# Optimization experiments

Measured on AMD Instinct MI355X. Metric: run time of the kernel, lower is better.

Reference implementation:

```python
import jax, jax.numpy as jnp
import numpy as np

NUM_HEADS = 8


def setup_inputs() -> dict:
    key = jax.random.key(0)
    ks = jax.random.split(key, 8)
    B, C, H, W = 8, 512, 64, 64
    s = 1.0 / np.sqrt(C)
    return {
        "guide": jax.random.normal(ks[0], (B, C), dtype=jnp.float32),
        "hidden_rep": jax.random.normal(ks[1], (B, C, H, W), dtype=jnp.float32),
        "Wq": jax.random.normal(ks[2], (C, C), dtype=jnp.float32) * s,
        "bq": jnp.zeros((C,), dtype=jnp.float32),
        "Wk": jax.random.normal(ks[3], (C, C), dtype=jnp.float32) * s,
        "bk": jnp.zeros((C,), dtype=jnp.float32),
        "Wv": jax.random.normal(ks[4], (C, C), dtype=jnp.float32) * s,
        "bv": jnp.zeros((C,), dtype=jnp.float32),
    }


def reference(guide, hidden_rep, Wq, bq, Wk, bk, Wv, bv):
    B, C, H, W = hidden_rep.shape
    nh = NUM_HEADS
    d = C // nh
    scale = 1.0 / (d ** 0.5)

    # hidden_rep: [B,C,H,W] -> [B, HW, C] (token-major, matching torch permute+reshape)
    hr = hidden_rep.transpose(0, 2, 3, 1).reshape(B, H * W, C)

    # guide is broadcast identically over all HW positions in the original;
    # the linear commutes with the broadcast, so compute once then broadcast.
    q_row = guide @ Wq.T + bq                                   # [B, C]
    q_tok = jnp.broadcast_to(q_row[:, None, :], (B, H * W, C))  # [B, HW, C]
    k_tok = hr @ Wk.T + bk                                      # [B, HW, C]
    v_tok = hr @ Wv.T + bv                                      # [B, HW, C]

    # Faithful replication of torch split_heads: view [B,HW,C] as [B,nh,d,H,W]
    # (this scrambles spatial/channel axes exactly as the original does),
    # then permute to [B, nh, H, W, d].
    def split_heads(x):
        return x.reshape(B, nh, d, H, W).transpose(0, 1, 3, 4, 2)

    q = split_heads(q_tok)  # [B, nh, H, W, d]
    k = split_heads(k_tok)
    v = split_heads(v_tok)

    # Row-wise attention: softmax over the width axis only.
    scores = jnp.einsum('bnhqd,bnhkd->bnhqk', q, k) * scale  # [B, nh, H, W, W]
    weights = jax.nn.softmax(scores, axis=-1)
    attended = jnp.einsum('bnhqk,bnhkd->bnhqd', weights, v)  # [B, nh, H, W, d]

    # permute(0,1,4,2,3) -> [B, nh, d, H, W] -> [B, C, H, W]
    return attended.transpose(0, 1, 4, 2, 3).reshape(B, C, H, W)
```

## Files before the change

### kernel.cpp

```cpp
#include <hip/hip_runtime.h>
#include <hip/hip_bf16.h>
#include <stdint.h>


typedef __attribute__((ext_vector_type(8))) short bf16x8_t;
typedef __attribute__((ext_vector_type(4))) float f32x4_t;

__device__ __forceinline__ unsigned short f2bf(float f) {
  unsigned int u = __float_as_uint(f);
  u += 0x7FFFu + ((u >> 16) & 1u);
  return (unsigned short)(u >> 16);
}

__device__ __forceinline__ void gload16(const unsigned short* g, void* lds) {
  __builtin_amdgcn_global_load_lds(
      (const __attribute__((address_space(1))) unsigned int*)g,
      (__attribute__((address_space(3))) unsigned int*)lds, 16, 0, 0);
}

__global__ __launch_bounds__(256) void k_wvb(const float* __restrict__ Wv,
                                             unsigned short* __restrict__ Wvb) {
  int gid = blockIdx.x * 256 + threadIdx.x;
  float4 v = ((const float4*)Wv)[gid];
  ushort4 o;
  o.x = f2bf(v.x); o.y = f2bf(v.y); o.z = f2bf(v.z); o.w = f2bf(v.w);
  ((ushort4*)Wvb)[gid] = o;
}

__global__ __launch_bounds__(256) void k_trans(const float* __restrict__ hid,
                                               unsigned short* __restrict__ XT,
                                               float* __restrict__ hrsum) {
  int bid = blockIdx.x;
  int cb = bid & 7, n = (bid >> 3) & 7, b = bid >> 6;
  int tid = threadIdx.x;
  __shared__ float T[64][65];
  __shared__ float hsred[64][8];

  for (int i = tid; i < 512; i += 256) ((float*)hsred)[i] = 0.f;

  float part[4][4];
#pragma unroll
  for (int m = 0; m < 4; ++m)
#pragma unroll
    for (int i = 0; i < 4; ++i) part[m][i] = 0.f;

  const int f4 = tid & 15;
  const int r0 = tid >> 4;
  const float* srcbase = hid + (size_t)(b * 512 + cb * 64) * 4096 + n * 512;
  unsigned short* xtbase = XT + (size_t)(b * 8 + n) * 512 * 512 + cb * 64;

  for (int jc = 0; jc < 8; ++jc) {
    __syncthreads();
#pragma unroll
    for (int m = 0; m < 4; ++m) {
      int r = r0 + 16 * m;
      float4 v = *(const float4*)(srcbase + (size_t)r * 4096 + jc * 64 + f4 * 4);
      T[r][f4 * 4 + 0] = v.x;  T[r][f4 * 4 + 1] = v.y;
      T[r][f4 * 4 + 2] = v.z;  T[r][f4 * 4 + 3] = v.w;
      part[m][0] += v.x; part[m][1] += v.y; part[m][2] += v.z; part[m][3] += v.w;
    }
    __syncthreads();
#pragma unroll
    for (int p = 0; p < 2; ++p) {
      int jl = (tid >> 3) + p * 32;
      int o = tid & 7;
      unsigned short t0 = f2bf(T[o * 8 + 0][jl]);
      unsigned short t1 = f2bf(T[o * 8 + 1][jl]);
      unsigned short t2 = f2bf(T[o * 8 + 2][jl]);
      unsigned short t3 = f2bf(T[o * 8 + 3][jl]);
      unsigned short t4 = f2bf(T[o * 8 + 4][jl]);
      unsigned short t5 = f2bf(T[o * 8 + 5][jl]);
      unsigned short t6 = f2bf(T[o * 8 + 6][jl]);
      unsigned short t7 = f2bf(T[o * 8 + 7][jl]);
      uint4 pk;
      pk.x = (unsigned)t0 | ((unsigned)t1 << 16);
      pk.y = (unsigned)t2 | ((unsigned)t3 << 16);
      pk.z = (unsigned)t4 | ((unsigned)t5 << 16);
      pk.w = (unsigned)t6 | ((unsigned)t7 << 16);
      *(uint4*)(xtbase + (size_t)(jc * 64 + jl) * 512 + o * 8) = pk;
    }
  }
  __syncthreads();
  {
    int gbase = (tid & 1) * 4;
#pragma unroll
    for (int m = 0; m < 4; ++m) {
      int r = r0 + 16 * m;
#pragma unroll
      for (int i = 0; i < 4; ++i) atomicAdd(&hsred[r][gbase + i], part[m][i]);
    }
  }
  __syncthreads();
  float* hout = hrsum + (size_t)(b * 8 + n) * 8 * 512 + cb * 64;
  for (int i = tid; i < 512; i += 256) {
    int g = i >> 6, r = i & 63;
    hout[(size_t)g * 512 + r] = hsred[r][g];
  }
}

__global__ __launch_bounds__(256) void k_k2(const float* __restrict__ hrsum,
                                            const float* __restrict__ Wk,
                                            const float* __restrict__ bk,
                                            const float* __restrict__ guide,
                                            const float* __restrict__ Wq,
                                            const float* __restrict__ bq,
                                            float* __restrict__ K2,
                                            float* __restrict__ qs) {
  int bid = blockIdx.x;
  int rt = bid >> 4, ct = bid & 15;
  bool isQ = (rt == 16);
  const float* A = isQ ? guide : (hrsum + (size_t)rt * 32 * 512);
  const float* Bm = isQ ? Wq : Wk;
  int arows = isQ ? 8 : 32;
  int tid = threadIdx.x;
  __shared__ float Ah[32][36];
  __shared__ float Bh[32][36];
  int r = tid >> 3, f = tid & 7;
  int oy = (tid >> 4) * 2, ox = (tid & 15) * 2;
  float a00 = 0.f, a01 = 0.f, a10 = 0.f, a11 = 0.f;

  for (int kc = 0; kc < 16; ++kc) {
    __syncthreads();
    float4 av = (r < arows) ? *(const float4*)(A + (size_t)r * 512 + kc * 32 + f * 4)
                            : make_float4(0.f, 0.f, 0.f, 0.f);
    *(float4*)(&Ah[r][f * 4]) = av;
    float4 bv = *(const float4*)(Bm + (size_t)(ct * 32 + r) * 512 + kc * 32 + f * 4);
    *(float4*)(&Bh[r][f * 4]) = bv;
    __syncthreads();
#pragma unroll
    for (int kk = 0; kk < 32; kk += 4) {
      float4 x0 = *(float4*)(&Ah[oy][kk]);
      float4 x1 = *(float4*)(&Ah[oy + 1][kk]);
      float4 y0 = *(float4*)(&Bh[ox][kk]);
      float4 y1 = *(float4*)(&Bh[ox + 1][kk]);
      a00 += x0.x * y0.x + x0.y * y0.y + x0.z * y0.z + x0.w * y0.w;
      a01 += x0.x * y1.x + x0.y * y1.y + x0.z * y1.z + x0.w * y1.w;
      a10 += x1.x * y0.x + x1.y * y0.y + x1.z * y0.z + x1.w * y0.w;
      a11 += x1.x * y1.x + x1.y * y1.y + x1.z * y1.z + x1.w * y1.w;
    }
  }
  int c0 = ct * 32 + ox;
  if (!isQ) {
    int row0 = rt * 32 + oy;
    K2[(size_t)row0 * 512 + c0]           = a00 + 64.f * bk[c0];
    K2[(size_t)row0 * 512 + c0 + 1]       = a01 + 64.f * bk[c0 + 1];
    K2[(size_t)(row0 + 1) * 512 + c0]     = a10 + 64.f * bk[c0];
    K2[(size_t)(row0 + 1) * 512 + c0 + 1] = a11 + 64.f * bk[c0 + 1];
  } else if (oy < 8) {
    const float scale = 0.125f;
    qs[(size_t)oy * 512 + c0]           = (a00 + bq[c0]) * scale;
    qs[(size_t)oy * 512 + c0 + 1]       = (a01 + bq[c0 + 1]) * scale;
    qs[(size_t)(oy + 1) * 512 + c0]     = (a10 + bq[c0]) * scale;
    qs[(size_t)(oy + 1) * 512 + c0 + 1] = (a11 + bq[c0 + 1]) * scale;
  }
}

__global__ __launch_bounds__(512, 4) void k_fused(
    const unsigned short* __restrict__ XT, const unsigned short* __restrict__ Wvb,
    const float* __restrict__ K2, const float* __restrict__ qs,
    const float* __restrict__ bv, float* __restrict__ out) {
  int bid = blockIdx.x;
  int g = bid & 7, slab = bid >> 3;
  int n = slab & 7, b = slab >> 3;
  int tid = threadIdx.x;
  int w = tid >> 6, l = tid & 63;
  int l15 = l & 15, l4 = l >> 4, lr = l >> 3, lc = l & 7;

  __shared__ __align__(16) unsigned char smem[77824];
  unsigned char* Al = smem;
  unsigned char* Bl = smem + 65536;
  float* K2l = (float*)(smem + 73728);
  float* bvl = (float*)(smem + 75776);

  if (tid < 128) {
    ((float4*)K2l)[tid] = ((const float4*)(K2 + (size_t)(slab * 8 + g) * 512))[tid];
  } else if (tid < 256) {
    ((float4*)bvl)[tid - 128] = ((const float4*)bv)[tid - 128];
  }

  const unsigned swzel = (unsigned)(lc ^ lr) << 3;
  const unsigned short* bsrc = XT + (size_t)slab * 512 * 512;

  f32x4_t acc[4][4];
#pragma unroll
  for (int i = 0; i < 4; ++i)
#pragma unroll
    for (int j = 0; j < 4; ++j) acc[i][j] = (f32x4_t){0.f, 0.f, 0.f, 0.f};

  const int myArow = w * 64;
  const int myBrow = w * 8;

  for (int kc = 0; kc < 8; ++kc) {
    if (kc) __syncthreads();
#pragma unroll
    for (int i = 0; i < 8; ++i) {
      int r = myArow + i * 8 + lr;
      gload16(Wvb + (size_t)r * 512 + kc * 64 + swzel, Al + (myArow + i * 8) * 128);
    }
    {
      int r = myBrow + lr;
      int j = 8 * r + g;
      gload16(bsrc + (size_t)j * 512 + kc * 64 + swzel, Bl + myBrow * 128);
    }
    __syncthreads();
#pragma unroll
    for (int ks = 0; ks < 2; ++ks) {
      unsigned colb = (unsigned)(ks * 64 + l4 * 16);
      bf16x8_t af[4], bfr[4];
#pragma unroll
      for (int mt = 0; mt < 4; ++mt) {
        unsigned row = (unsigned)(myArow + mt * 16 + l15);
        af[mt] = *(const bf16x8_t*)(Al + row * 128 + (colb ^ ((row & 7) << 4)));
      }
#pragma unroll
      for (int nt = 0; nt < 4; ++nt) {
        unsigned row = (unsigned)(nt * 16 + l15);
        bfr[nt] = *(const bf16x8_t*)(Bl + row * 128 + (colb ^ ((row & 7) << 4)));
      }
#pragma unroll
      for (int mt = 0; mt < 4; ++mt)
#pragma unroll
        for (int nt = 0; nt < 4; ++nt)
          acc[mt][nt] = __builtin_amdgcn_mfma_f32_16x16x32_bf16(
              af[mt], bfr[nt], acc[mt][nt], 0, 0, 0);
    }
  }

  __syncthreads();
  unsigned char* Vl = Al;
#pragma unroll
  for (int nt = 0; nt < 4; ++nt) {
    unsigned dd = (unsigned)(nt * 16 + l15);
    unsigned swz = (dd & 7) << 4;
#pragma unroll
    for (int mt = 0; mt < 4; ++mt) {
      int c0 = w * 64 + mt * 16 + l4 * 4;
      float4 bq4 = *(const float4*)(bvl + c0);
      float v0 = acc[mt][nt][0] + bq4.x;
      float v1 = acc[mt][nt][1] + bq4.y;
      float v2 = acc[mt][nt][2] + bq4.z;
      float v3 = acc[mt][nt][3] + bq4.w;
      uint2 pk;
      pk.x = (unsigned)f2bf(v0) | ((unsigned)f2bf(v1) << 16);
      pk.y = (unsigned)f2bf(v2) | ((unsigned)f2bf(v3) << 16);
      *(uint2*)(Vl + dd * 1024 + (((unsigned)(c0 * 2)) ^ swz)) = pk;
    }
  }
  __syncthreads();

  const int e = w;
  float alpha = qs[(size_t)b * 512 + e * 64 + l];
  float mmax = -3.0e38f;
#pragma unroll 8
  for (int kk = 0; kk < 64; ++kk)
    mmax = fmaxf(mmax, alpha * K2l[e * 64 + kk]);
  float ssum = 0.f;
#pragma unroll 8
  for (int kk = 0; kk < 64; ++kk)
    ssum += __expf(alpha * K2l[e * 64 + kk] - mmax);
  float inv = 1.0f / ssum;

  f32x4_t acc2[4][4];
#pragma unroll
  for (int i = 0; i < 4; ++i)
#pragma unroll
    for (int j = 0; j < 4; ++j) acc2[i][j] = (f32x4_t){0.f, 0.f, 0.f, 0.f};

#pragma unroll
  for (int ks = 0; ks < 2; ++ks) {
    bf16x8_t va[4];
#pragma unroll
    for (int mt = 0; mt < 4; ++mt) {
      unsigned dd = (unsigned)(mt * 16 + l15);
      unsigned colb = (unsigned)(e * 128 + ks * 64 + l4 * 16);
      va[mt] = *(const bf16x8_t*)(Vl + dd * 1024 + (colb ^ ((dd & 7) << 4)));
    }
    int kk0 = ks * 32 + l4 * 8;
    float4 be0 = *(float4*)(&K2l[e * 64 + kk0]);
    float4 be1 = *(float4*)(&K2l[e * 64 + kk0 + 4]);
    bf16x8_t pb[4];
#pragma unroll
    for (int nt = 0; nt < 4; ++nt) {
      int qq = nt * 16 + l15;
      float aq = __shfl(alpha, qq);
      float mq = __shfl(mmax, qq);
      float iq = __shfl(inv, qq);
      bf16x8_t p;
      p[0] = (short)f2bf(__expf(aq * be0.x - mq) * iq);
      p[1] = (short)f2bf(__expf(aq * be0.y - mq) * iq);
      p[2] = (short)f2bf(__expf(aq * be0.z - mq) * iq);
      p[3] = (short)f2bf(__expf(aq * be0.w - mq) * iq);
      p[4] = (short)f2bf(__expf(aq * be1.x - mq) * iq);
      p[5] = (short)f2bf(__expf(aq * be1.y - mq) * iq);
      p[6] = (short)f2bf(__expf(aq * be1.z - mq) * iq);
      p[7] = (short)f2bf(__expf(aq * be1.w - mq) * iq);
      pb[nt] = p;
    }
#pragma unroll
    for (int mt = 0; mt < 4; ++mt)
#pragma unroll
      for (int nt = 0; nt < 4; ++nt)
        acc2[mt][nt] = __builtin_amdgcn_mfma_f32_16x16x32_bf16(
            va[mt], pb[nt], acc2[mt][nt], 0, 0, 0);
  }

#pragma unroll
  for (int mt = 0; mt < 4; ++mt) {
#pragma unroll
    for (int r = 0; r < 4; ++r) {
      int dd = mt * 16 + l4 * 4 + r;
      size_t base = (((size_t)(b * 512 + n * 64 + dd)) * 64 + (g * 8 + e)) * 64;
#pragma unroll
      for (int nt = 0; nt < 4; ++nt)
        out[base + nt * 16 + l15] = acc2[mt][nt][r];
    }
  }
}

extern "C" void kernel_launch(void* const* d_in, const int* in_sizes, int n_in,
                              void* d_out, int out_size, void* d_ws, size_t ws_size,
                              hipStream_t stream) {
  const float* guide = (const float*)d_in[0];
  const float* hid   = (const float*)d_in[1];
  const float* Wq    = (const float*)d_in[2];
  const float* bq    = (const float*)d_in[3];
  const float* Wk    = (const float*)d_in[4];
  const float* bk    = (const float*)d_in[5];
  const float* Wv    = (const float*)d_in[6];
  const float* bv    = (const float*)d_in[7];
  float* out = (float*)d_out;

  char* ws = (char*)d_ws;
  unsigned short* XT  = (unsigned short*)(ws);
  unsigned short* Wvb = (unsigned short*)(ws + 33554432);
  float* hrsum        = (float*)(ws + 34078720);
  float* K2           = (float*)(ws + 35127296);
  float* qs           = (float*)(ws + 36175872);

  k_wvb<<<256, 256, 0, stream>>>(Wv, Wvb);
  k_trans<<<512, 256, 0, stream>>>(hid, XT, hrsum);
  k_k2<<<272, 256, 0, stream>>>(hrsum, Wk, bk, guide, Wq, bq, K2, qs);
  k_fused<<<512, 512, 0, stream>>>(XT, Wvb, K2, qs, bv, out);
}
```

Measured before the change: 98.45 us.

## Double-buffer fused GEMM staging with async LDS loads and merge Wv conversion kernel

Folds the Wv-to-bf16 conversion into the transpose kernel as 16 extra blocks, saving one launch. The fused kernel now double-buffers its A/B LDS tiles, using vmcnt waits and raw barriers so the next K chunk's global-to-LDS loads overlap the current chunk's MFMA work. K2 and bias are also fetched with async LDS loads. The larger shared memory (about 148KB) lowers occupancy to fewer blocks per CU, which may offset the latency hiding.

```diff
diff --git a/kernel.cpp b/kernel.cpp
--- a/kernel.cpp
+++ b/kernel.cpp
@@ -12,27 +12,32 @@
   return (unsigned short)(u >> 16);
 }
 
-__device__ __forceinline__ void gload16(const unsigned short* g, void* lds) {
+__device__ __forceinline__ void gload16(const void* g, void* lds) {
   __builtin_amdgcn_global_load_lds(
       (const __attribute__((address_space(1))) unsigned int*)g,
       (__attribute__((address_space(3))) unsigned int*)lds, 16, 0, 0);
 }
 
-__global__ __launch_bounds__(256) void k_wvb(const float* __restrict__ Wv,
-                                             unsigned short* __restrict__ Wvb) {
-  int gid = blockIdx.x * 256 + threadIdx.x;
-  float4 v = ((const float4*)Wv)[gid];
-  ushort4 o;
-  o.x = f2bf(v.x); o.y = f2bf(v.y); o.z = f2bf(v.z); o.w = f2bf(v.w);
-  ((ushort4*)Wvb)[gid] = o;
-}
-
 __global__ __launch_bounds__(256) void k_trans(const float* __restrict__ hid,
                                                unsigned short* __restrict__ XT,
-                                               float* __restrict__ hrsum) {
+                                               float* __restrict__ hrsum,
+                                               const float* __restrict__ Wv,
+                                               unsigned short* __restrict__ Wvb) {
   int bid = blockIdx.x;
+  int tid = threadIdx.x;
+  if (bid >= 512) {
+    int blk = bid - 512;
+#pragma unroll
+    for (int i = 0; i < 16; ++i) {
+      int idx = blk * 4096 + i * 256 + tid;
+      float4 v = ((const float4*)Wv)[idx];
+      ushort4 o;
+      o.x = f2bf(v.x); o.y = f2bf(v.y); o.z = f2bf(v.z); o.w = f2bf(v.w);
+      ((ushort4*)Wvb)[idx] = o;
+    }
+    return;
+  }
   int cb = bid & 7, n = (bid >> 3) & 7, b = bid >> 6;
-  int tid = threadIdx.x;
   __shared__ float T[64][65];
   __shared__ float hsred[64][8];
 
@@ -155,7 +160,7 @@
   }
 }
 
-__global__ __launch_bounds__(512, 4) void k_fused(
+__global__ __launch_bounds__(512, 2) void k_fused(
     const unsigned short* __restrict__ XT, const unsigned short* __restrict__ Wvb,
     const float* __restrict__ K2, const float* __restrict__ qs,
     const float* __restrict__ bv, float* __restrict__ out) {
@@ -166,68 +171,85 @@
   int w = tid >> 6, l = tid & 63;
   int l15 = l & 15, l4 = l >> 4, lr = l >> 3, lc = l & 7;
 
-  __shared__ __align__(16) unsigned char smem[77824];
-  unsigned char* Al = smem;
-  unsigned char* Bl = smem + 65536;
-  float* K2l = (float*)(smem + 73728);
-  float* bvl = (float*)(smem + 75776);
-
-  if (tid < 128) {
-    ((float4*)K2l)[tid] = ((const float4*)(K2 + (size_t)(slab * 8 + g) * 512))[tid];
-  } else if (tid < 256) {
-    ((float4*)bvl)[tid - 128] = ((const float4*)bv)[tid - 128];
-  }
-
-  const unsigned swzel = (unsigned)(lc ^ lr) << 3;
+  __shared__ __align__(16) unsigned char smem[151552];
+  float* K2l = (float*)(smem + 147456);
+  float* bvl = (float*)(smem + 149504);
+
+  const unsigned swzel = (unsigned)((lc ^ lr) << 3);
   const unsigned short* bsrc = XT + (size_t)slab * 512 * 512;
-
-  f32x4_t acc[4][4];
-#pragma unroll
-  for (int i = 0; i < 4; ++i)
-#pragma unroll
-    for (int j = 0; j < 4; ++j) acc[i][j] = (f32x4_t){0.f, 0.f, 0.f, 0.f};
-
   const int myArow = w * 64;
   const int myBrow = w * 8;
 
+  if (w < 2) {
+    gload16(K2 + (size_t)(slab * 8 + g) * 512 + w * 256 + l * 4,
+            (unsigned char*)K2l + w * 1024);
+  } else if (w < 4) {
+    gload16(bv + (w - 2) * 256 + l * 4, (unsigned char*)bvl + (w - 2) * 1024);
+  }
+
+#define STAGE(kc, buf)                                                          \
+  do {                                                                          \
+    unsigned char* Ab_ = smem + (buf)*65536;                                    \
+    unsigned char* Bb_ = smem + 131072 + (buf)*8192;                            \
+    _Pragma("unroll")                                                           \
+    for (int i_ = 0; i_ < 8; ++i_) {                                            \
+      int r_ = myArow + i_ * 8 + lr;                                            \
+      gload16(Wvb + (size_t)r_ * 512 + (kc)*64 + swzel,                         \
+              Ab_ + (myArow + i_ * 8) * 128);                                   \
+    }                                                                           \
+    int rb_ = myBrow + lr;                                                      \
+    gload16(bsrc + (size_t)(8 * rb_ + g) * 512 + (kc)*64 + swzel,               \
+            Bb_ + myBrow * 128);                                                \
+  } while (0)
+
+  f32x4_t acc[4][4];
+#pragma unroll
+  for (int i = 0; i < 4; ++i)
+#pragma unroll
+    for (int j = 0; j < 4; ++j) acc[i][j] = (f32x4_t){0.f, 0.f, 0.f, 0.f};
+
+  STAGE(0, 0);
+  STAGE(1, 1);
+
+#pragma unroll
   for (int kc = 0; kc < 8; ++kc) {
-    if (kc) __syncthreads();
-#pragma unroll
-    for (int i = 0; i < 8; ++i) {
-      int r = myArow + i * 8 + lr;
-      gload16(Wvb + (size_t)r * 512 + kc * 64 + swzel, Al + (myArow + i * 8) * 128);
-    }
+    if (kc < 7) asm volatile("s_waitcnt vmcnt(9)" ::: "memory");
+    else        asm volatile("s_waitcnt vmcnt(0)" ::: "memory");
+    __builtin_amdgcn_s_barrier();
     {
-      int r = myBrow + lr;
-      int j = 8 * r + g;
-      gload16(bsrc + (size_t)j * 512 + kc * 64 + swzel, Bl + myBrow * 128);
-    }
-    __syncthreads();
-#pragma unroll
-    for (int ks = 0; ks < 2; ++ks) {
-      unsigned colb = (unsigned)(ks * 64 + l4 * 16);
-      bf16x8_t af[4], bfr[4];
-#pragma unroll
-      for (int mt = 0; mt < 4; ++mt) {
-        unsigned row = (unsigned)(myArow + mt * 16 + l15);
-        af[mt] = *(const bf16x8_t*)(Al + row * 128 + (colb ^ ((row & 7) << 4)));
+      unsigned char* Ab = smem + (kc & 1) * 65536;
+      unsigned char* Bb = smem + 131072 + (kc & 1) * 8192;
+#pragma unroll
+      for (int ks = 0; ks < 2; ++ks) {
+        unsigned colb = (unsigned)(ks * 64 + l4 * 16);
+        bf16x8_t af[4], bfr[4];
+#pragma unroll
+        for (int mt = 0; mt < 4; ++mt) {
+          unsigned row = (unsigned)(myArow + mt * 16 + l15);
+          af[mt] = *(const bf16x8_t*)(Ab + row * 128 + (colb ^ ((row & 7) << 4)));
+        }
+#pragma unroll
+        for (int nt = 0; nt < 4; ++nt) {
+          unsigned row = (unsigned)(nt * 16 + l15);
+          bfr[nt] = *(const bf16x8_t*)(Bb + row * 128 + (colb ^ ((row & 7) << 4)));
+        }
+#pragma unroll
+        for (int mt = 0; mt < 4; ++mt)
+#pragma unroll
+          for (int nt = 0; nt < 4; ++nt)
+            acc[mt][nt] = __builtin_amdgcn_mfma_f32_16x16x32_bf16(
+                af[mt], bfr[nt], acc[mt][nt], 0, 0, 0);
       }
-#pragma unroll
-      for (int nt = 0; nt < 4; ++nt) {
-        unsigned row = (unsigned)(nt * 16 + l15);
-        bfr[nt] = *(const bf16x8_t*)(Bl + row * 128 + (colb ^ ((row & 7) << 4)));
-      }
-#pragma unroll
-      for (int mt = 0; mt < 4; ++mt)
-#pragma unroll
-        for (int nt = 0; nt < 4; ++nt)
-          acc[mt][nt] = __builtin_amdgcn_mfma_f32_16x16x32_bf16(
-              af[mt], bfr[nt], acc[mt][nt], 0, 0, 0);
-    }
-  }
-
-  __syncthreads();
-  unsigned char* Vl = Al;
+    }
+    __builtin_amdgcn_s_barrier();
+    if (kc < 6) {
+      if ((kc & 1) == 0) STAGE(kc + 2, 0);
+      else               STAGE(kc + 2, 1);
+    }
+  }
+#undef STAGE
+
+  unsigned char* Vl = smem;
 #pragma unroll
   for (int nt = 0; nt < 4; ++nt) {
     unsigned dd = (unsigned)(nt * 16 + l15);
@@ -337,8 +359,7 @@
   float* K2           = (float*)(ws + 35127296);
   float* qs           = (float*)(ws + 36175872);
 
-  k_wvb<<<256, 256, 0, stream>>>(Wv, Wvb);
-  k_trans<<<512, 256, 0, stream>>>(hid, XT, hrsum);
+  k_trans<<<528, 256, 0, stream>>>(hid, XT, hrsum, Wv, Wvb);
   k_k2<<<272, 256, 0, stream>>>(hrsum, Wk, bk, guide, Wq, bq, K2, qs);
   k_fused<<<512, 512, 0, stream>>>(XT, Wvb, K2, qs, bv, out);
 }
```

Result: faster. 96.20 us (-2.3%).
